# Performance work log

Measured on AMD Instinct MI355X. Metric: run time of the kernel, lower is better.

The kernel has to match this reference:

```python
import jax, jax.numpy as jnp
import numpy as np

VOCAB = 65535
EMB = 1024
CTX = 1024
B = 32
HID = 4 * EMB


def setup_inputs() -> dict:
    key = jax.random.key(0)
    ks = jax.random.split(key, 20)
    s = 0.02
    inp = {
        "idx": jax.random.randint(ks[0], (B, 1), 0, VOCAB),
        "key_cache": jax.random.normal(ks[1], (B, CTX - 1, EMB), jnp.float32),
        "value_cache": jax.random.normal(ks[2], (B, CTX - 1, EMB), jnp.float32),
        "emb_table": jax.random.normal(ks[3], (VOCAB, EMB), jnp.float32) * s,
        "pos_table": jax.random.normal(ks[4], (CTX, EMB), jnp.float32) * s,
        "Wk": jax.random.normal(ks[5], (EMB, EMB), jnp.float32) * s,
        "bk": jnp.zeros((EMB,), jnp.float32),
        "Wv": jax.random.normal(ks[6], (EMB, EMB), jnp.float32) * s,
        "bv": jnp.zeros((EMB,), jnp.float32),
        "Wq": jax.random.normal(ks[7], (EMB, EMB), jnp.float32) * s,
        "bq": jnp.zeros((EMB,), jnp.float32),
        "W1": jax.random.normal(ks[8], (EMB, HID), jnp.float32) * s,
        "b1": jnp.zeros((HID,), jnp.float32),
        "W2": jax.random.normal(ks[9], (HID, EMB), jnp.float32) * s,
        "b2": jnp.zeros((EMB,), jnp.float32),
        "Wl": jax.random.normal(ks[10], (EMB, VOCAB), jnp.float32) * s,
        "bl": jnp.zeros((VOCAB,), jnp.float32),
    }
    return inp


def reference(idx, key_cache, value_cache, emb_table, pos_table,
              Wk, bk, Wv, bv, Wq, bq, W1, b1, W2, b2, Wl, bl):
    # token + position embeddings (seq_len=1, positions = arange(1) = [0])
    tok = emb_table[idx]                      # [B, 1, D]
    pos = pos_table[:1][None, :, :]           # [1, 1, D]
    x = tok + pos                             # [B, 1, D]

    # cache truncation to last context_size-1 steps (no-op here at 1023)
    kc = key_cache[:, -(CTX - 1):, :]
    vc = value_cache[:, -(CTX - 1):, :]

    # single-head attention with KV cache
    k_new = x @ Wk + bk                       # [B, 1, D]
    v_new = x @ Wv + bv
    q_new = x @ Wq + bq
    keys = jnp.concatenate([kc, k_new], axis=1)    # [B, S, D]
    values = jnp.concatenate([vc, v_new], axis=1)  # [B, S, D]
    scale = 1.0 / jnp.sqrt(jnp.asarray(EMB, x.dtype))
    scores = jnp.einsum("bqd,bsd->bqs", q_new, keys) * scale  # [B, 1, S]
    probs = jax.nn.softmax(scores, axis=-1)
    attn_out = jnp.einsum("bqs,bsd->bqd", probs, values)      # [B, 1, D]

    # feed-forward (exact GELU, matching torch nn.GELU default)
    h = jax.nn.gelu(attn_out @ W1 + b1, approximate=False)
    ffn_out = h @ W2 + b2                     # [B, 1, D]

    logits = ffn_out @ Wl + bl                # [B, 1, VOCAB]
    return logits
```

## Files before the change

kernel.cpp:

```cpp
#include <hip/hip_runtime.h>
#include <cstddef>

#define BATCH 32
#define EMBD 1024
#define SCTX 1023
#define CTXF 1024
#define HIDD 4096
#define VOC 65535

__global__ void embed_kernel(const int* __restrict__ idx, const float* __restrict__ emb,
                             const float* __restrict__ pos, float* __restrict__ x) {
  int b = blockIdx.x, t = threadIdx.x;
  const float4* er = (const float4*)(emb + (size_t)idx[b] * EMBD);
  const float4* pr = (const float4*)pos;
  float4 e = er[t], p = pr[t];
  ((float4*)(x + (size_t)b * EMBD))[t] = make_float4(e.x + p.x, e.y + p.y, e.z + p.z, e.w + p.w);
}

__global__ void skgemm_qkv(const float* __restrict__ X,
                           const float* __restrict__ Wk, const float* __restrict__ Wv,
                           const float* __restrict__ Wq,
                           float* __restrict__ Pout, int chunk) {
  const float* __restrict__ W = (blockIdx.z == 0) ? Wk : (blockIdx.z == 1) ? Wv : Wq;
  int j = blockIdx.x * 256 + threadIdx.x;
  int p = blockIdx.y;
  int nch = gridDim.y;
  float acc[BATCH];
#pragma unroll
  for (int b = 0; b < BATCH; ++b) acc[b] = 0.f;
  int i0 = p * chunk;
#pragma unroll 8
  for (int i = i0; i < i0 + chunk; ++i) {
    float w = W[(size_t)i * EMBD + j];
#pragma unroll
    for (int b = 0; b < BATCH; ++b) acc[b] = fmaf(X[b * EMBD + i], w, acc[b]);
  }
#pragma unroll
  for (int b = 0; b < BATCH; ++b)
    Pout[((size_t)(blockIdx.z * nch + p) * BATCH + b) * EMBD + j] = acc[b];
}

__global__ void reduce_qkv(const float* __restrict__ part, int P,
                           const float* __restrict__ bk, const float* __restrict__ bv,
                           const float* __restrict__ bq,
                           float* __restrict__ kout, float* __restrict__ vout,
                           float* __restrict__ qout) {
  int z = blockIdx.y;
  int m = blockIdx.x * 256 + threadIdx.x;
  float s = 0.f;
  for (int p = 0; p < P; ++p) s += part[(size_t)(z * P + p) * (BATCH * EMBD) + m];
  const float* bias = (z == 0) ? bk : (z == 1) ? bv : bq;
  float* out = (z == 0) ? kout : (z == 1) ? vout : qout;
  out[m] = s + bias[m & (EMBD - 1)];
}

template <int BB>
__global__ void skgemm(const float* __restrict__ X, const float* __restrict__ W,
                       float* __restrict__ Pout, int N, int K, int chunk) {
  int j = blockIdx.x * 256 + threadIdx.x;
  int p = blockIdx.y;
  float acc[BB];
#pragma unroll
  for (int b = 0; b < BB; ++b) acc[b] = 0.f;
  int i0 = p * chunk, i1 = i0 + chunk;
#pragma unroll 8
  for (int i = i0; i < i1; ++i) {
    float w = W[(size_t)i * N + j];
#pragma unroll
    for (int b = 0; b < BB; ++b) acc[b] = fmaf(X[b * K + i], w, acc[b]);
  }
#pragma unroll
  for (int b = 0; b < BB; ++b) Pout[((size_t)p * BB + b) * N + j] = acc[b];
}

__global__ void reduce_ep(const float* __restrict__ part, int P,
                          const float* __restrict__ bias, float* __restrict__ out,
                          int total, int mask, int act) {
  int m = blockIdx.x * 256 + threadIdx.x;
  if (m >= total) return;
  float s = 0.f;
  for (int p = 0; p < P; ++p) s += part[(size_t)p * total + m];
  if (bias) s += bias[m & mask];
  if (act == 1) s = 0.5f * s * (1.f + erff(s * 0.70710678118654752f));
  out[m] = s;
}

__global__ void scores_kernel(const float* __restrict__ q, const float* __restrict__ kcache,
                              const float* __restrict__ knew, float* __restrict__ scores) {
  int b = blockIdx.y;
  int wave = threadIdx.x >> 6, lane = threadIdx.x & 63;
  const float* qb = q + (size_t)b * EMBD;
  float4 qf[4];
#pragma unroll
  for (int r = 0; r < 4; ++r) qf[r] = *(const float4*)(qb + r * 256 + lane * 4);
  int sbase = blockIdx.x * 16 + wave * 4;
  const float* kr[4];
  float acc[4] = {0.f, 0.f, 0.f, 0.f};
#pragma unroll
  for (int it = 0; it < 4; ++it) {
    int s = sbase + it;
    kr[it] = (s < SCTX) ? (kcache + ((size_t)b * SCTX + s) * EMBD)
                        : (knew + (size_t)b * EMBD);
  }
#pragma unroll
  for (int r = 0; r < 4; ++r) {
#pragma unroll
    for (int it = 0; it < 4; ++it) {
      float4 kf = *(const float4*)(kr[it] + r * 256 + lane * 4);
      acc[it] += qf[r].x * kf.x + qf[r].y * kf.y + qf[r].z * kf.z + qf[r].w * kf.w;
    }
  }
#pragma unroll
  for (int it = 0; it < 4; ++it) {
    float a = acc[it];
#pragma unroll
    for (int m = 32; m > 0; m >>= 1) a += __shfl_xor(a, m, 64);
    if (lane == 0) scores[(size_t)b * CTXF + sbase + it] = a * 0.03125f;
  }
}

__global__ void softmax_kernel(float* __restrict__ sc) {
  int b = blockIdx.x;
  int t = threadIdx.x;
  __shared__ float red[16];
  float v = sc[(size_t)b * CTXF + t];
  float m = v;
#pragma unroll
  for (int d = 32; d > 0; d >>= 1) m = fmaxf(m, __shfl_xor(m, d, 64));
  if ((t & 63) == 0) red[t >> 6] = m;
  __syncthreads();
  float bm = red[0];
#pragma unroll
  for (int w = 1; w < 16; ++w) bm = fmaxf(bm, red[w]);
  float e = expf(v - bm);
  __syncthreads();
  float s = e;
#pragma unroll
  for (int d = 32; d > 0; d >>= 1) s += __shfl_xor(s, d, 64);
  if ((t & 63) == 0) red[t >> 6] = s;
  __syncthreads();
  float bs = 0.f;
#pragma unroll
  for (int w = 0; w < 16; ++w) bs += red[w];
  sc[(size_t)b * CTXF + t] = e / bs;
}

__global__ void pv_kernel(const float* __restrict__ probs, const float* __restrict__ vcache,
                          const float* __restrict__ vnew, float* __restrict__ part) {
  int b = blockIdx.y;
  int p = blockIdx.x;
  int t = threadIdx.x;
  float acc[4] = {0.f, 0.f, 0.f, 0.f};
  int s0 = p * 32;
#pragma unroll 4
  for (int s = s0; s < s0 + 32; ++s) {
    float pr = probs[(size_t)b * CTXF + s];
    const float* vrow = (s < SCTX) ? (vcache + ((size_t)b * SCTX + s) * EMBD)
                                   : (vnew + (size_t)b * EMBD);
#pragma unroll
    for (int r = 0; r < 4; ++r) acc[r] = fmaf(pr, vrow[t + r * 256], acc[r]);
  }
#pragma unroll
  for (int r = 0; r < 4; ++r) part[((size_t)p * BATCH + b) * EMBD + t + r * 256] = acc[r];
}

__global__ __launch_bounds__(256) void logits_v3(const float* __restrict__ X,
                                                 const float* __restrict__ Wl,
                                                 float* __restrict__ part) {
  __shared__ float xt[256][BATCH];
  int t = threadIdx.x;
  int p = blockIdx.y;
  int q0 = p * 256;
  for (int m = t; m < 256 * BATCH; m += 256) {
    int i = m >> 5, b = m & 31;
    xt[i][b] = X[b * EMBD + q0 + i];
  }
  __syncthreads();

  int jb = blockIdx.x * 512;
  int j0 = jb + t;
  int j1 = jb + 256 + t;
  bool v1 = (j1 < VOC);
  float acc0[BATCH], acc1[BATCH];
#pragma unroll
  for (int b = 0; b < BATCH; ++b) { acc0[b] = 0.f; acc1[b] = 0.f; }

  const float* wp = Wl + (size_t)q0 * VOC;
#pragma unroll 4
  for (int i = 0; i < 256; ++i) {
    float w0 = wp[(size_t)i * VOC + j0];
    float w1 = v1 ? wp[(size_t)i * VOC + j1] : 0.f;
#pragma unroll
    for (int b = 0; b < BATCH; ++b) {
      float xv = xt[i][b];
      acc0[b] = fmaf(xv, w0, acc0[b]);
      acc1[b] = fmaf(xv, w1, acc1[b]);
    }
  }
#pragma unroll
  for (int b = 0; b < BATCH; ++b) {
    part[((size_t)p * BATCH + b) * VOC + j0] = acc0[b];
    if (v1) part[((size_t)p * BATCH + b) * VOC + j1] = acc1[b];
  }
}

__global__ void logits_reduce(const float* __restrict__ part, const float* __restrict__ bl,
                              float* __restrict__ out) {
  size_t m = (size_t)blockIdx.x * 256 + threadIdx.x;
  if (m >= (size_t)BATCH * VOC) return;
  int j = (int)(m % VOC);
  float s = 0.f;
#pragma unroll
  for (int p = 0; p < 4; ++p) s += part[(size_t)p * BATCH * VOC + m];
  out[m] = s + bl[j];
}

__global__ void logits_splitb(const float* __restrict__ X, const float* __restrict__ Wl,
                              const float* __restrict__ bl, float* __restrict__ out) {
  int j = blockIdx.x * 256 + threadIdx.x;
  if (j >= VOC) return;
  int b0 = blockIdx.y * 16;
  float acc[16];
#pragma unroll
  for (int b = 0; b < 16; ++b) acc[b] = 0.f;
#pragma unroll 8
  for (int i = 0; i < EMBD; ++i) {
    float w = Wl[(size_t)i * VOC + j];
#pragma unroll
    for (int b = 0; b < 16; ++b) acc[b] = fmaf(X[(b0 + b) * EMBD + i], w, acc[b]);
  }
  float bb = bl[j];
#pragma unroll
  for (int b = 0; b < 16; ++b) out[(size_t)(b0 + b) * VOC + j] = acc[b] + bb;
}

extern "C" void kernel_launch(void* const* d_in, const int* in_sizes, int n_in,
                              void* d_out, int out_size, void* d_ws, size_t ws_size,
                              hipStream_t stream) {
  const int* idx = (const int*)d_in[0];
  const float* key_cache = (const float*)d_in[1];
  const float* value_cache = (const float*)d_in[2];
  const float* emb_table = (const float*)d_in[3];
  const float* pos_table = (const float*)d_in[4];
  const float* Wk = (const float*)d_in[5];
  const float* bk = (const float*)d_in[6];
  const float* Wv = (const float*)d_in[7];
  const float* bv = (const float*)d_in[8];
  const float* Wq = (const float*)d_in[9];
  const float* bq = (const float*)d_in[10];
  const float* W1 = (const float*)d_in[11];
  const float* b1 = (const float*)d_in[12];
  const float* W2 = (const float*)d_in[13];
  const float* b2 = (const float*)d_in[14];
  const float* Wl = (const float*)d_in[15];
  const float* bl = (const float*)d_in[16];
  float* out = (float*)d_out;

  float* ws = (float*)d_ws;
  float* x    = ws;
  float* k    = ws + 32768;
  float* v    = ws + 65536;
  float* q    = ws + 98304;
  float* prob = ws + 131072;
  float* attn = ws + 163840;
  float* h    = ws + 196608;
  float* ffn  = ws + 327680;
  float* part = ws + 360448;

  size_t partCap = (ws_size / 4 > 360448) ? ws_size / 4 - 360448 : 0;

  embed_kernel<<<dim3(BATCH), 256, 0, stream>>>(idx, emb_table, pos_table, x);

  int QC = (partCap >= (size_t)3 * 32 * BATCH * EMBD) ? 32 : 8;
  skgemm_qkv<<<dim3(4, QC, 3), 256, 0, stream>>>(x, Wk, Wv, Wq, part, EMBD / QC);
  reduce_qkv<<<dim3(128, 3), 256, 0, stream>>>(part, QC, bk, bv, bq, k, v, q);

  scores_kernel<<<dim3(64, BATCH), 256, 0, stream>>>(q, key_cache, k, prob);
  softmax_kernel<<<dim3(BATCH), 1024, 0, stream>>>(prob);
  pv_kernel<<<dim3(32, BATCH), 256, 0, stream>>>(prob, value_cache, v, part);
  reduce_ep<<<dim3(128), 256, 0, stream>>>(part, 32, nullptr, attn, BATCH * EMBD, 0, 0);

  int F1C = (partCap >= (size_t)16 * BATCH * HIDD) ? 16 : 8;
  skgemm<BATCH><<<dim3(16, F1C), 256, 0, stream>>>(attn, W1, part, HIDD, EMBD, EMBD / F1C);
  reduce_ep<<<dim3(512), 256, 0, stream>>>(part, F1C, b1, h, BATCH * HIDD, HIDD - 1, 1);

  int F2C = (partCap >= (size_t)64 * BATCH * EMBD) ? 64 : 32;
  skgemm<BATCH><<<dim3(4, F2C), 256, 0, stream>>>(h, W2, part, EMBD, HIDD, HIDD / F2C);
  reduce_ep<<<dim3(128), 256, 0, stream>>>(part, F2C, b2, ffn, BATCH * EMBD, EMBD - 1, 0);

  if (partCap >= (size_t)4 * BATCH * VOC) {
    logits_v3<<<dim3(128, 4), 256, 0, stream>>>(ffn, Wl, part);
    logits_reduce<<<dim3(8192), 256, 0, stream>>>(part, bl, out);
  } else {
    logits_splitb<<<dim3(256, 2), 256, 0, stream>>>(ffn, Wl, bl, out);
  }
}
```

Before: 297.3 us.

## Fuse attention into split-softmax kernels, vectorize reductions, raise split-K counts

Replaces the separate scores, softmax and PV kernels with a flash-decoding style pair: each block computes scores for a 32-position chunk, a local softmax with max and sum, and the partial PV, and a second kernel rescales and combines the chunks. This removes a launch and the global round-trip of the probability matrix. All reduction kernels are switched to float4 loads and stores, the split-K counts for the FFN GEMMs are doubled when workspace allows, and the logits loop unroll is increased. The larger split counts raise partial-sum traffic, and the workspace layout shifts, so the large-split paths depend on enough scratch space being available.

```diff
diff --git a/kernel.cpp b/kernel.cpp
--- a/kernel.cpp
+++ b/kernel.cpp
@@ -7,6 +7,8 @@
 #define CTXF 1024
 #define HIDD 4096
 #define VOC 65535
+#define CH 32
+#define NCH 32
 
 __global__ void embed_kernel(const int* __restrict__ idx, const float* __restrict__ emb,
                              const float* __restrict__ pos, float* __restrict__ x) {
@@ -40,18 +42,23 @@
     Pout[((size_t)(blockIdx.z * nch + p) * BATCH + b) * EMBD + j] = acc[b];
 }
 
-__global__ void reduce_qkv(const float* __restrict__ part, int P,
-                           const float* __restrict__ bk, const float* __restrict__ bv,
-                           const float* __restrict__ bq,
-                           float* __restrict__ kout, float* __restrict__ vout,
-                           float* __restrict__ qout) {
+__global__ void reduce_qkv4(const float* __restrict__ part, int P,
+                            const float* __restrict__ bk, const float* __restrict__ bv,
+                            const float* __restrict__ bq,
+                            float* __restrict__ kout, float* __restrict__ vout,
+                            float* __restrict__ qout) {
   int z = blockIdx.y;
-  int m = blockIdx.x * 256 + threadIdx.x;
-  float s = 0.f;
-  for (int p = 0; p < P; ++p) s += part[(size_t)(z * P + p) * (BATCH * EMBD) + m];
+  int m4 = blockIdx.x * 256 + threadIdx.x;
+  float4 s = make_float4(0.f, 0.f, 0.f, 0.f);
+  for (int p = 0; p < P; ++p) {
+    float4 v = ((const float4*)part)[(size_t)(z * P + p) * (BATCH * EMBD / 4) + m4];
+    s.x += v.x; s.y += v.y; s.z += v.z; s.w += v.w;
+  }
   const float* bias = (z == 0) ? bk : (z == 1) ? bv : bq;
   float* out = (z == 0) ? kout : (z == 1) ? vout : qout;
-  out[m] = s + bias[m & (EMBD - 1)];
+  float4 bb = *(const float4*)(bias + ((m4 * 4) & (EMBD - 1)));
+  s.x += bb.x; s.y += bb.y; s.z += bb.z; s.w += bb.w;
+  ((float4*)out)[m4] = s;
 }
 
 template <int BB>
@@ -73,95 +80,119 @@
   for (int b = 0; b < BB; ++b) Pout[((size_t)p * BB + b) * N + j] = acc[b];
 }
 
-__global__ void reduce_ep(const float* __restrict__ part, int P,
-                          const float* __restrict__ bias, float* __restrict__ out,
-                          int total, int mask, int act) {
-  int m = blockIdx.x * 256 + threadIdx.x;
-  if (m >= total) return;
-  float s = 0.f;
-  for (int p = 0; p < P; ++p) s += part[(size_t)p * total + m];
-  if (bias) s += bias[m & mask];
-  if (act == 1) s = 0.5f * s * (1.f + erff(s * 0.70710678118654752f));
-  out[m] = s;
-}
-
-__global__ void scores_kernel(const float* __restrict__ q, const float* __restrict__ kcache,
-                              const float* __restrict__ knew, float* __restrict__ scores) {
-  int b = blockIdx.y;
+__global__ void reduce_ep4(const float* __restrict__ part, int P,
+                           const float* __restrict__ bias, float* __restrict__ out,
+                           int total4, int mask, int act) {
+  int m4 = blockIdx.x * 256 + threadIdx.x;
+  if (m4 >= total4) return;
+  float4 s = make_float4(0.f, 0.f, 0.f, 0.f);
+  for (int p = 0; p < P; ++p) {
+    float4 v = ((const float4*)part)[(size_t)p * total4 + m4];
+    s.x += v.x; s.y += v.y; s.z += v.z; s.w += v.w;
+  }
+  if (bias) {
+    float4 bb = *(const float4*)(bias + ((m4 * 4) & mask));
+    s.x += bb.x; s.y += bb.y; s.z += bb.z; s.w += bb.w;
+  }
+  if (act == 1) {
+    s.x = 0.5f * s.x * (1.f + erff(s.x * 0.70710678118654752f));
+    s.y = 0.5f * s.y * (1.f + erff(s.y * 0.70710678118654752f));
+    s.z = 0.5f * s.z * (1.f + erff(s.z * 0.70710678118654752f));
+    s.w = 0.5f * s.w * (1.f + erff(s.w * 0.70710678118654752f));
+  }
+  ((float4*)out)[m4] = s;
+}
+
+__global__ __launch_bounds__(256) void attnA(const float* __restrict__ q,
+                                             const float* __restrict__ kcache,
+                                             const float* __restrict__ knew,
+                                             const float* __restrict__ vcache,
+                                             const float* __restrict__ vnew,
+                                             float* __restrict__ opart,
+                                             float* __restrict__ ml) {
+  int b = blockIdx.y, c = blockIdx.x;
   int wave = threadIdx.x >> 6, lane = threadIdx.x & 63;
+  __shared__ float sc[CH], pexp[CH];
   const float* qb = q + (size_t)b * EMBD;
   float4 qf[4];
 #pragma unroll
   for (int r = 0; r < 4; ++r) qf[r] = *(const float4*)(qb + r * 256 + lane * 4);
-  int sbase = blockIdx.x * 16 + wave * 4;
-  const float* kr[4];
+  int s0 = c * CH;
+#pragma unroll
+  for (int g = 0; g < 2; ++g) {
+    int sbase = s0 + wave * 8 + g * 4;
+    const float* kr[4];
+    float acc[4] = {0.f, 0.f, 0.f, 0.f};
+#pragma unroll
+    for (int it = 0; it < 4; ++it) {
+      int s = sbase + it;
+      kr[it] = (s < SCTX) ? (kcache + ((size_t)b * SCTX + s) * EMBD)
+                          : (knew + (size_t)b * EMBD);
+    }
+#pragma unroll
+    for (int r = 0; r < 4; ++r) {
+#pragma unroll
+      for (int it = 0; it < 4; ++it) {
+        float4 kf = *(const float4*)(kr[it] + r * 256 + lane * 4);
+        acc[it] += qf[r].x * kf.x + qf[r].y * kf.y + qf[r].z * kf.z + qf[r].w * kf.w;
+      }
+    }
+#pragma unroll
+    for (int it = 0; it < 4; ++it) {
+      float a = acc[it];
+#pragma unroll
+      for (int m = 32; m > 0; m >>= 1) a += __shfl_xor(a, m, 64);
+      if (lane == 0) sc[sbase - s0 + it] = a * 0.03125f;
+    }
+  }
+  __syncthreads();
+  float m = sc[0];
+#pragma unroll
+  for (int s = 1; s < CH; ++s) m = fmaxf(m, sc[s]);
+  if (threadIdx.x < CH) pexp[threadIdx.x] = expf(sc[threadIdx.x] - m);
+  __syncthreads();
+  if (threadIdx.x == 0) {
+    float l = 0.f;
+#pragma unroll
+    for (int s = 0; s < CH; ++s) l += pexp[s];
+    ml[((size_t)c * BATCH + b) * 2] = m;
+    ml[((size_t)c * BATCH + b) * 2 + 1] = l;
+  }
+  int t = threadIdx.x;
+  float acc2[4] = {0.f, 0.f, 0.f, 0.f};
+#pragma unroll 4
+  for (int s = 0; s < CH; ++s) {
+    float pr = pexp[s];
+    const float* vrow = (s0 + s < SCTX) ? (vcache + ((size_t)b * SCTX + s0 + s) * EMBD)
+                                        : (vnew + (size_t)b * EMBD);
+#pragma unroll
+    for (int r = 0; r < 4; ++r) acc2[r] = fmaf(pr, vrow[t + r * 256], acc2[r]);
+  }
+#pragma unroll
+  for (int r = 0; r < 4; ++r)
+    opart[((size_t)c * BATCH + b) * EMBD + t + r * 256] = acc2[r];
+}
+
+__global__ void attnB(const float* __restrict__ opart, const float* __restrict__ ml,
+                      float* __restrict__ attn) {
+  int b = blockIdx.x, t = threadIdx.x;
+  float M = ml[(size_t)b * 2];
+#pragma unroll
+  for (int c = 1; c < NCH; ++c) M = fmaxf(M, ml[((size_t)c * BATCH + b) * 2]);
+  float L = 0.f;
+#pragma unroll
+  for (int c = 0; c < NCH; ++c)
+    L += expf(ml[((size_t)c * BATCH + b) * 2] - M) * ml[((size_t)c * BATCH + b) * 2 + 1];
+  float inv = 1.f / L;
   float acc[4] = {0.f, 0.f, 0.f, 0.f};
-#pragma unroll
-  for (int it = 0; it < 4; ++it) {
-    int s = sbase + it;
-    kr[it] = (s < SCTX) ? (kcache + ((size_t)b * SCTX + s) * EMBD)
-                        : (knew + (size_t)b * EMBD);
-  }
-#pragma unroll
-  for (int r = 0; r < 4; ++r) {
-#pragma unroll
-    for (int it = 0; it < 4; ++it) {
-      float4 kf = *(const float4*)(kr[it] + r * 256 + lane * 4);
-      acc[it] += qf[r].x * kf.x + qf[r].y * kf.y + qf[r].z * kf.z + qf[r].w * kf.w;
-    }
-  }
-#pragma unroll
-  for (int it = 0; it < 4; ++it) {
-    float a = acc[it];
-#pragma unroll
-    for (int m = 32; m > 0; m >>= 1) a += __shfl_xor(a, m, 64);
-    if (lane == 0) scores[(size_t)b * CTXF + sbase + it] = a * 0.03125f;
-  }
-}
-
-__global__ void softmax_kernel(float* __restrict__ sc) {
-  int b = blockIdx.x;
-  int t = threadIdx.x;
-  __shared__ float red[16];
-  float v = sc[(size_t)b * CTXF + t];
-  float m = v;
-#pragma unroll
-  for (int d = 32; d > 0; d >>= 1) m = fmaxf(m, __shfl_xor(m, d, 64));
-  if ((t & 63) == 0) red[t >> 6] = m;
-  __syncthreads();
-  float bm = red[0];
-#pragma unroll
-  for (int w = 1; w < 16; ++w) bm = fmaxf(bm, red[w]);
-  float e = expf(v - bm);
-  __syncthreads();
-  float s = e;
-#pragma unroll
-  for (int d = 32; d > 0; d >>= 1) s += __shfl_xor(s, d, 64);
-  if ((t & 63) == 0) red[t >> 6] = s;
-  __syncthreads();
-  float bs = 0.f;
-#pragma unroll
-  for (int w = 0; w < 16; ++w) bs += red[w];
-  sc[(size_t)b * CTXF + t] = e / bs;
-}
-
-__global__ void pv_kernel(const float* __restrict__ probs, const float* __restrict__ vcache,
-                          const float* __restrict__ vnew, float* __restrict__ part) {
-  int b = blockIdx.y;
-  int p = blockIdx.x;
-  int t = threadIdx.x;
-  float acc[4] = {0.f, 0.f, 0.f, 0.f};
-  int s0 = p * 32;
-#pragma unroll 4
-  for (int s = s0; s < s0 + 32; ++s) {
-    float pr = probs[(size_t)b * CTXF + s];
-    const float* vrow = (s < SCTX) ? (vcache + ((size_t)b * SCTX + s) * EMBD)
-                                   : (vnew + (size_t)b * EMBD);
-#pragma unroll
-    for (int r = 0; r < 4; ++r) acc[r] = fmaf(pr, vrow[t + r * 256], acc[r]);
-  }
-#pragma unroll
-  for (int r = 0; r < 4; ++r) part[((size_t)p * BATCH + b) * EMBD + t + r * 256] = acc[r];
+  for (int c = 0; c < NCH; ++c) {
+    float wc = expf(ml[((size_t)c * BATCH + b) * 2] - M);
+#pragma unroll
+    for (int r = 0; r < 4; ++r)
+      acc[r] = fmaf(wc, opart[((size_t)c * BATCH + b) * EMBD + t + r * 256], acc[r]);
+  }
+#pragma unroll
+  for (int r = 0; r < 4; ++r) attn[(size_t)b * EMBD + t + r * 256] = acc[r] * inv;
 }
 
 __global__ __launch_bounds__(256) void logits_v3(const float* __restrict__ X,
@@ -186,7 +217,7 @@
   for (int b = 0; b < BATCH; ++b) { acc0[b] = 0.f; acc1[b] = 0.f; }
 
   const float* wp = Wl + (size_t)q0 * VOC;
-#pragma unroll 4
+#pragma unroll 8
   for (int i = 0; i < 256; ++i) {
     float w0 = wp[(size_t)i * VOC + j0];
     float w1 = v1 ? wp[(size_t)i * VOC + j1] : 0.f;
@@ -204,15 +235,24 @@
   }
 }
 
-__global__ void logits_reduce(const float* __restrict__ part, const float* __restrict__ bl,
-                              float* __restrict__ out) {
-  size_t m = (size_t)blockIdx.x * 256 + threadIdx.x;
-  if (m >= (size_t)BATCH * VOC) return;
-  int j = (int)(m % VOC);
-  float s = 0.f;
-#pragma unroll
-  for (int p = 0; p < 4; ++p) s += part[(size_t)p * BATCH * VOC + m];
-  out[m] = s + bl[j];
+__global__ void logits_reduce4(const float* __restrict__ part, const float* __restrict__ bl,
+                               float* __restrict__ out) {
+  unsigned m4 = blockIdx.x * 256 + threadIdx.x;
+  const unsigned N4 = (unsigned)BATCH * VOC / 4;
+  if (m4 >= N4) return;
+  float4 s = make_float4(0.f, 0.f, 0.f, 0.f);
+#pragma unroll
+  for (int p = 0; p < 4; ++p) {
+    float4 v = ((const float4*)part)[(size_t)p * N4 + m4];
+    s.x += v.x; s.y += v.y; s.z += v.z; s.w += v.w;
+  }
+  unsigned e0 = m4 * 4u;
+  unsigned j = e0 % (unsigned)VOC;
+  unsigned j1 = j + 1 >= VOC ? j + 1 - VOC : j + 1;
+  unsigned j2 = j + 2 >= VOC ? j + 2 - VOC : j + 2;
+  unsigned j3 = j + 3 >= VOC ? j + 3 - VOC : j + 3;
+  s.x += bl[j]; s.y += bl[j1]; s.z += bl[j2]; s.w += bl[j3];
+  ((float4*)out)[m4] = s;
 }
 
 __global__ void logits_splitb(const float* __restrict__ X, const float* __restrict__ Wl,
@@ -257,40 +297,40 @@
   float* out = (float*)d_out;
 
   float* ws = (float*)d_ws;
-  float* x    = ws;
-  float* k    = ws + 32768;
-  float* v    = ws + 65536;
-  float* q    = ws + 98304;
-  float* prob = ws + 131072;
-  float* attn = ws + 163840;
-  float* h    = ws + 196608;
-  float* ffn  = ws + 327680;
-  float* part = ws + 360448;
-
-  size_t partCap = (ws_size / 4 > 360448) ? ws_size / 4 - 360448 : 0;
+  float* x     = ws;
+  float* k     = ws + 32768;
+  float* v     = ws + 65536;
+  float* q     = ws + 98304;
+  float* attn  = ws + 131072;
+  float* h     = ws + 163840;
+  float* ffn   = ws + 294912;
+  float* opart = ws + 327680;
+  float* ml    = ws + 1376256;
+  float* part  = ws + 1378304;
+
+  size_t wsf = ws_size / 4;
+  size_t partCap = (wsf > 1378304) ? wsf - 1378304 : 0;
 
   embed_kernel<<<dim3(BATCH), 256, 0, stream>>>(idx, emb_table, pos_table, x);
 
   int QC = (partCap >= (size_t)3 * 32 * BATCH * EMBD) ? 32 : 8;
   skgemm_qkv<<<dim3(4, QC, 3), 256, 0, stream>>>(x, Wk, Wv, Wq, part, EMBD / QC);
-  reduce_qkv<<<dim3(128, 3), 256, 0, stream>>>(part, QC, bk, bv, bq, k, v, q);
-
-  scores_kernel<<<dim3(64, BATCH), 256, 0, stream>>>(q, key_cache, k, prob);
-  softmax_kernel<<<dim3(BATCH), 1024, 0, stream>>>(prob);
-  pv_kernel<<<dim3(32, BATCH), 256, 0, stream>>>(prob, value_cache, v, part);
-  reduce_ep<<<dim3(128), 256, 0, stream>>>(part, 32, nullptr, attn, BATCH * EMBD, 0, 0);
-
-  int F1C = (partCap >= (size_t)16 * BATCH * HIDD) ? 16 : 8;
+  reduce_qkv4<<<dim3(32, 3), 256, 0, stream>>>(part, QC, bk, bv, bq, k, v, q);
+
+  attnA<<<dim3(NCH, BATCH), 256, 0, stream>>>(q, key_cache, k, value_cache, v, opart, ml);
+  attnB<<<dim3(BATCH), 256, 0, stream>>>(opart, ml, attn);
+
+  int F1C = (partCap >= (size_t)32 * BATCH * HIDD) ? 32 : 8;
   skgemm<BATCH><<<dim3(16, F1C), 256, 0, stream>>>(attn, W1, part, HIDD, EMBD, EMBD / F1C);
-  reduce_ep<<<dim3(512), 256, 0, stream>>>(part, F1C, b1, h, BATCH * HIDD, HIDD - 1, 1);
-
-  int F2C = (partCap >= (size_t)64 * BATCH * EMBD) ? 64 : 32;
+  reduce_ep4<<<dim3(128), 256, 0, stream>>>(part, F1C, b1, h, BATCH * HIDD / 4, HIDD - 1, 1);
+
+  int F2C = (partCap >= (size_t)128 * BATCH * EMBD) ? 128 : 32;
   skgemm<BATCH><<<dim3(4, F2C), 256, 0, stream>>>(h, W2, part, EMBD, HIDD, HIDD / F2C);
-  reduce_ep<<<dim3(128), 256, 0, stream>>>(part, F2C, b2, ffn, BATCH * EMBD, EMBD - 1, 0);
+  reduce_ep4<<<dim3(32), 256, 0, stream>>>(part, F2C, b2, ffn, BATCH * EMBD / 4, EMBD - 1, 0);
 
   if (partCap >= (size_t)4 * BATCH * VOC) {
     logits_v3<<<dim3(128, 4), 256, 0, stream>>>(ffn, Wl, part);
-    logits_reduce<<<dim3(8192), 256, 0, stream>>>(part, bl, out);
+    logits_reduce4<<<dim3(2048), 256, 0, stream>>>(part, bl, out);
   } else {
     logits_splitb<<<dim3(256, 2), 256, 0, stream>>>(ffn, Wl, bl, out);
   }
```

Result: slower. 337.3 us (+13.4%).
